# Kernel tuning notes

Measured on AMD Instinct MI355X. Metric: run time of the kernel, lower is better.

Reference implementation:

```python
import jax, jax.numpy as jnp
import numpy as np

N_NODES = 100000
N_EDGES = 1600000
IN_F = 128
HID = 128
N_CLASSES = 2
N_GRAPHS = 512


def setup_inputs() -> dict:
    key = jax.random.key(0)
    ks = jax.random.split(key, 12)
    x = jax.random.normal(ks[0], (N_NODES, IN_F), dtype=jnp.float32)
    edge_index = jax.random.randint(ks[1], (2, N_EDGES), 0, N_NODES, dtype=jnp.int64)
    batch = jnp.sort(jax.random.randint(ks[2], (N_NODES,), 0, N_GRAPHS, dtype=jnp.int64))
    s_in = 1.0 / np.sqrt(IN_F)
    s_h = 1.0 / np.sqrt(HID)
    return {
        "x": x,
        "edge_index": edge_index,
        "batch": batch,
        "W1": jax.random.normal(ks[3], (IN_F, HID), dtype=jnp.float32) * s_in,
        "b1": jnp.zeros((HID,), dtype=jnp.float32),
        "W2": jax.random.normal(ks[4], (HID, HID), dtype=jnp.float32) * s_h,
        "b2": jnp.zeros((HID,), dtype=jnp.float32),
        "W3": jax.random.normal(ks[5], (HID, HID), dtype=jnp.float32) * s_h,
        "b3": jnp.zeros((HID,), dtype=jnp.float32),
        "Wl": jax.random.normal(ks[6], (HID, N_CLASSES), dtype=jnp.float32) * s_h,
        "bl": jnp.zeros((N_CLASSES,), dtype=jnp.float32),
    }


def reference(x, edge_index, batch, W1, b1, W2, b2, W3, b3, Wl, bl):
    n = x.shape[0]
    src, dst = edge_index[0], edge_index[1]
    # GCNConv adds self-loops and applies symmetric normalization D^-1/2 (A+I) D^-1/2
    loop = jnp.arange(n, dtype=src.dtype)
    src_f = jnp.concatenate([src, loop])  # [E+N]
    dst_f = jnp.concatenate([dst, loop])
    deg = jax.ops.segment_sum(jnp.ones_like(src_f, dtype=x.dtype), dst_f, num_segments=n)
    dis = jax.lax.rsqrt(jnp.maximum(deg, 1.0))  # deg >= 1 due to self-loops
    norm = dis[src_f] * dis[dst_f]  # [E+N]

    def conv(h, W, b):
        h = h @ W                                    # [N, H]
        msg = h[src_f] * norm[:, None]               # gather + scale  [E+N, H]
        agg = jax.ops.segment_sum(msg, dst_f, num_segments=n)  # scatter-add
        return agg + b

    h = jax.nn.relu(conv(x, W1, b1))
    h = jax.nn.relu(conv(h, W2, b2))
    h = conv(h, W3, b3)
    # global_mean_pool over graph ids
    sums = jax.ops.segment_sum(h, batch, num_segments=N_GRAPHS)        # [G, H]
    cnt = jax.ops.segment_sum(jnp.ones((n,), h.dtype), batch, num_segments=N_GRAPHS)
    pooled = sums / jnp.maximum(cnt, 1.0)[:, None]
    # dropout p=0.5 is identity in eval mode
    return pooled @ Wl + bl
```

## Files before the change

kernel.cpp:

```cpp
#include <hip/hip_runtime.h>

#define NF 128
#define NFU 64
#define BW 128
#define KMAX 1024
#define CAP 3072
#define CHUNK 8192

typedef __attribute__((ext_vector_type(8))) short bf16x8;
typedef __attribute__((ext_vector_type(4))) float f32x4;
union U4S8 { uint4 u; bf16x8 s; };

__global__ void detect_kernel(const int* __restrict__ ei, int ne, int* __restrict__ mode) {
    if (threadIdx.x == 0 && blockIdx.x == 0) {
        int step = ne / 32; if (step < 1) step = 1;
        int all0 = 1;
        for (int k = 0; k < 16; ++k) {
            int idx = 2 * k * step + 1;
            if (ei[idx] != 0) { all0 = 0; break; }
        }
        *mode = all0;
    }
}

__global__ __launch_bounds__(256) void hist_kernel(const int* __restrict__ ei, int ne, int n,
                                                   const int* __restrict__ mode, int* __restrict__ btotal,
                                                   int K) {
    __shared__ int hist[KMAX];
    int m = *mode;
    int tid = threadIdx.x;
    for (int k = tid; k < K; k += 256) hist[k] = 0;
    __syncthreads();
    int base = blockIdx.x * CHUNK;
    int end = min(base + CHUNK, ne);
    for (int e = base + tid; e < end; e += 256) {
        int dst = m ? ei[2 * (ne + e)] : ei[ne + e];
        if ((unsigned)dst < (unsigned)n) atomicAdd(&hist[dst >> 7], 1);
    }
    __syncthreads();
    for (int k = tid; k < K; k += 256)
        if (hist[k]) atomicAdd(&btotal[k], hist[k]);
}

__global__ __launch_bounds__(1024) void scanK(const int* __restrict__ btotal, int* __restrict__ bbase,
                                              int* __restrict__ gcur, int K) {
    __shared__ int sm[1024];
    int tid = threadIdx.x;
    int v = (tid < K) ? btotal[tid] : 0;
    sm[tid] = v;
    __syncthreads();
    for (int off = 1; off < 1024; off <<= 1) {
        int t = (tid >= off) ? sm[tid - off] : 0;
        __syncthreads();
        sm[tid] += t;
        __syncthreads();
    }
    if (tid < K) {
        int excl = sm[tid] - v;
        bbase[tid] = excl;
        gcur[tid] = excl;
        if (tid == K - 1) bbase[K] = sm[tid];
    }
}

__global__ __launch_bounds__(256) void scatter_kernel(const int* __restrict__ ei, int ne, int n,
                                                      const int* __restrict__ mode, int* __restrict__ gcur,
                                                      uint2* __restrict__ pairbuf, int K) {
    __shared__ int cur[KMAX];
    int m = *mode;
    int tid = threadIdx.x;
    for (int k = tid; k < K; k += 256) cur[k] = 0;
    __syncthreads();
    int base = blockIdx.x * CHUNK;
    int end = min(base + CHUNK, ne);
    for (int e = base + tid; e < end; e += 256) {
        int dst = m ? ei[2 * (ne + e)] : ei[ne + e];
        if ((unsigned)dst < (unsigned)n) atomicAdd(&cur[dst >> 7], 1);
    }
    __syncthreads();
    for (int k = tid; k < K; k += 256) {
        int c = cur[k];
        cur[k] = c ? atomicAdd(&gcur[k], c) : 0;
    }
    __syncthreads();
    for (int e = base + tid; e < end; e += 256) {
        int src = m ? ei[2 * e] : ei[e];
        int dst = m ? ei[2 * (ne + e)] : ei[ne + e];
        if ((unsigned)dst >= (unsigned)n || (unsigned)src >= (unsigned)n) continue;
        int pos = atomicAdd(&cur[dst >> 7], 1);
        pairbuf[pos] = make_uint2((unsigned)src, (unsigned)dst);
    }
}

__global__ __launch_bounds__(256) void sort_kernel(const uint2* __restrict__ pairbuf,
                                                   const int* __restrict__ bbase,
                                                   int* __restrict__ rowptr, float* __restrict__ dis,
                                                   int* __restrict__ col, int n, int K) {
    __shared__ uint2 spair[CAP];
    __shared__ int lcol[CAP];
    __shared__ int dcnt[BW];
    __shared__ int pref[BW];
    int tid = threadIdx.x;
    int b = blockIdx.x;
    int r0 = b * BW;
    int base = bbase[b];
    int end = bbase[b + 1];
    int cntb = end - base;
    if (cntb > CAP) cntb = CAP;

    for (int i = tid; i < cntb; i += 256) spair[i] = pairbuf[base + i];
    if (tid < BW) dcnt[tid] = 0;
    __syncthreads();
    for (int i = tid; i < cntb; i += 256) atomicAdd(&dcnt[spair[i].y & (BW - 1)], 1);
    __syncthreads();
    if (tid < BW) pref[tid] = dcnt[tid];
    __syncthreads();
    for (int off = 1; off < BW; off <<= 1) {
        int t = (tid < BW && tid >= off) ? pref[tid - off] : 0;
        __syncthreads();
        if (tid < BW) pref[tid] += t;
        __syncthreads();
    }
    if (tid < BW) {
        int d = r0 + tid;
        if (d < n) {
            int excl = pref[tid] - dcnt[tid];
            rowptr[d] = base + excl;
            dis[d] = rsqrtf((float)(dcnt[tid] + 1));
        }
    }
    if (b == K - 1 && tid == 0) rowptr[n] = end;
    if (tid < BW) dcnt[tid] = pref[tid] - dcnt[tid];
    __syncthreads();
    for (int i = tid; i < cntb; i += 256) {
        int slot = atomicAdd(&dcnt[spair[i].y & (BW - 1)], 1);
        if (slot < CAP) lcol[slot] = (int)spair[i].x;
    }
    __syncthreads();
    for (int i = tid; i < cntb; i += 256) col[base + i] = lcol[i];
}

__device__ inline unsigned pack_bf16(float a, float b) {
    unsigned ua = __float_as_uint(a), ub = __float_as_uint(b);
    ua = (ua + 0x7fffu + ((ua >> 16) & 1u)) >> 16;
    ub = (ub + 0x7fffu + ((ub >> 16) & 1u)) >> 16;
    return ua | (ub << 16);
}
__device__ inline float bflo(unsigned u) { return __uint_as_float(u << 16); }
__device__ inline float bfhi(unsigned u) { return __uint_as_float(u & 0xFFFF0000u); }

__global__ __launch_bounds__(256) void wprep_kernel(const float* __restrict__ W, uint4* __restrict__ Wb) {
    int tid = threadIdx.x;
#pragma unroll
    for (int it = 0; it < 8; ++it) {
        int item = it * 256 + tid;
        int lane = item & 63;
        int kbjt = item >> 6;
        int kb = kbjt & 3, jt = kbjt >> 2;
        int k0 = kb * 32 + (lane >> 4) * 8;
        int j = jt * 16 + (lane & 15);
        unsigned p[4];
#pragma unroll
        for (int q = 0; q < 4; ++q)
            p[q] = pack_bf16(W[(size_t)(k0 + 2 * q) * NF + j], W[(size_t)(k0 + 2 * q + 1) * NF + j]);
        Wb[item] = make_uint4(p[0], p[1], p[2], p[3]);
    }
}

__global__ __launch_bounds__(256) void mm_mfma_kernel(const void* __restrict__ A, int a_fp32,
                                                      const uint4* __restrict__ Wb,
                                                      const float* __restrict__ dis,
                                                      unsigned* __restrict__ hs, int n) {
    int tid = threadIdx.x;
    int wave = tid >> 6, lane = tid & 63;
    int r0 = blockIdx.x * 64 + wave * 16;
    if (r0 >= n) return;
    int lrow = lane & 15, lk = lane >> 4;
    int arow = min(r0 + lrow, n - 1);

    f32x4 acc[8];
#pragma unroll
    for (int j = 0; j < 8; ++j) acc[j] = (f32x4){0.f, 0.f, 0.f, 0.f};

    U4S8 af[4];
    if (a_fp32) {
        const float* Af = (const float*)A;
#pragma unroll
        for (int kb = 0; kb < 4; ++kb) {
            const float* p = Af + (size_t)arow * NF + kb * 32 + lk * 8;
            float4 x0 = *(const float4*)p;
            float4 x1 = *(const float4*)(p + 4);
            af[kb].u = make_uint4(pack_bf16(x0.x, x0.y), pack_bf16(x0.z, x0.w),
                                  pack_bf16(x1.x, x1.y), pack_bf16(x1.z, x1.w));
        }
    } else {
        const unsigned* Ab = (const unsigned*)A;
#pragma unroll
        for (int kb = 0; kb < 4; ++kb)
            af[kb].u = *(const uint4*)(Ab + (size_t)arow * NFU + kb * 16 + lk * 4);
    }

#pragma unroll
    for (int kb = 0; kb < 4; ++kb) {
#pragma unroll
        for (int jt = 0; jt < 8; ++jt) {
            U4S8 wf;
            wf.u = Wb[(jt * 4 + kb) * 64 + lane];
            acc[jt] = __builtin_amdgcn_mfma_f32_16x16x32_bf16(wf.s, af[kb].s, acc[jt], 0, 0, 0);
        }
    }

    if (r0 + lrow < n) {
        float dv = dis[r0 + lrow];
        unsigned* orow = hs + (size_t)(r0 + lrow) * NFU;
#pragma unroll
        for (int jt = 0; jt < 8; ++jt) {
            unsigned p0 = pack_bf16(acc[jt][0] * dv, acc[jt][1] * dv);
            unsigned p1 = pack_bf16(acc[jt][2] * dv, acc[jt][3] * dv);
            *(uint2*)(orow + jt * 8 + lk * 2) = make_uint2(p0, p1);
        }
    }
}

__global__ __launch_bounds__(256) void spmm_kernel(const unsigned* __restrict__ hs, const int* __restrict__ rowptr,
                                                   const int* __restrict__ col, const float* __restrict__ dis,
                                                   const float* __restrict__ b, unsigned* __restrict__ outb,
                                                   int n, int do_relu) {
    int wid = (blockIdx.x * blockDim.x + threadIdx.x) >> 6;
    int lane = threadIdx.x & 63;
    if (wid >= n) return;
    int s = rowptr[wid], e = rowptr[wid + 1];
    int deg = e - s;
    int group = lane >> 4, fl = lane & 15;

    float acc[8];
    if (group == 0) {
        uint4 sv = *(const uint4*)(hs + (size_t)wid * NFU + fl * 4);
        acc[0] = bflo(sv.x); acc[1] = bfhi(sv.x);
        acc[2] = bflo(sv.y); acc[3] = bfhi(sv.y);
        acc[4] = bflo(sv.z); acc[5] = bfhi(sv.z);
        acc[6] = bflo(sv.w); acc[7] = bfhi(sv.w);
    } else {
#pragma unroll
        for (int k = 0; k < 8; ++k) acc[k] = 0.f;
    }

    int m64 = min(deg, 64);
    int cidx = (lane < m64) ? col[s + lane] : 0;

    for (int j0 = 0; j0 < m64; j0 += 4) {
        int c = __shfl(cidx, j0 + group);
        if (j0 + group < m64) {
            uint4 v = *(const uint4*)(hs + (size_t)c * NFU + fl * 4);
            acc[0] += bflo(v.x); acc[1] += bfhi(v.x);
            acc[2] += bflo(v.y); acc[3] += bfhi(v.y);
            acc[4] += bflo(v.z); acc[5] += bfhi(v.z);
            acc[6] += bflo(v.w); acc[7] += bfhi(v.w);
        }
    }
    for (int i = s + 64 + group; i < e; i += 4) {
        int c = col[i];
        uint4 v = *(const uint4*)(hs + (size_t)c * NFU + fl * 4);
        acc[0] += bflo(v.x); acc[1] += bfhi(v.x);
        acc[2] += bflo(v.y); acc[3] += bfhi(v.y);
        acc[4] += bflo(v.z); acc[5] += bfhi(v.z);
        acc[6] += bflo(v.w); acc[7] += bfhi(v.w);
    }

#pragma unroll
    for (int k = 0; k < 8; ++k) {
        acc[k] += __shfl_xor(acc[k], 16);
        acc[k] += __shfl_xor(acc[k], 32);
    }

    if (lane < 16) {
        float d = dis[wid];
        float4 bb0 = *(const float4*)(b + fl * 8);
        float4 bb1 = *(const float4*)(b + fl * 8 + 4);
        float o[8];
        o[0] = fmaf(d, acc[0], bb0.x); o[1] = fmaf(d, acc[1], bb0.y);
        o[2] = fmaf(d, acc[2], bb0.z); o[3] = fmaf(d, acc[3], bb0.w);
        o[4] = fmaf(d, acc[4], bb1.x); o[5] = fmaf(d, acc[5], bb1.y);
        o[6] = fmaf(d, acc[6], bb1.z); o[7] = fmaf(d, acc[7], bb1.w);
        if (do_relu) {
#pragma unroll
            for (int k = 0; k < 8; ++k) o[k] = fmaxf(o[k], 0.f);
        }
        unsigned q0 = pack_bf16(o[0], o[1]);
        unsigned q1 = pack_bf16(o[2], o[3]);
        unsigned q2 = pack_bf16(o[4], o[5]);
        unsigned q3 = pack_bf16(o[6], o[7]);
        *(uint4*)(outb + (size_t)wid * NFU + fl * 4) = make_uint4(q0, q1, q2, q3);
    }
}

__global__ void gbounds_kernel(const int* __restrict__ batch, const int* __restrict__ mode,
                               int* __restrict__ gstart, int n, int G) {
    int m = *mode;
    int i = blockIdx.x * blockDim.x + threadIdx.x;
    if (i >= n) return;
    int g1 = m ? batch[2 * i] : batch[i];
    int g2 = (i == n - 1) ? G : (m ? batch[2 * (i + 1)] : batch[i + 1]);
    if ((unsigned)g1 > (unsigned)G) g1 = G;
    if ((unsigned)g2 > (unsigned)G) g2 = G;
    if (i == 0) for (int g = 0; g <= g1; ++g) gstart[g] = 0;
    for (int g = g1 + 1; g <= g2; ++g) gstart[g] = i + 1;
}

__global__ __launch_bounds__(256) void poolhead_kernel(const unsigned* __restrict__ h, const int* __restrict__ gstart,
                                                       const float* __restrict__ Wl, const float* __restrict__ bl,
                                                       float* __restrict__ out, int G) {
    __shared__ float sacc[16][16][8];
    int g = blockIdx.x;
    int s = gstart[g], e = gstart[g + 1];
    int tid = threadIdx.x;
    int rg = tid >> 4, fl = tid & 15;

    float acc[8] = {0.f, 0.f, 0.f, 0.f, 0.f, 0.f, 0.f, 0.f};
    for (int i = s + rg; i < e; i += 16) {
        uint4 v = *(const uint4*)(h + (size_t)i * NFU + fl * 4);
        acc[0] += bflo(v.x); acc[1] += bfhi(v.x);
        acc[2] += bflo(v.y); acc[3] += bfhi(v.y);
        acc[4] += bflo(v.z); acc[5] += bfhi(v.z);
        acc[6] += bflo(v.w); acc[7] += bfhi(v.w);
    }
#pragma unroll
    for (int k = 0; k < 8; ++k) sacc[rg][fl][k] = acc[k];
    __syncthreads();
    if (tid < 16) {
        float t[8] = {0.f, 0.f, 0.f, 0.f, 0.f, 0.f, 0.f, 0.f};
        for (int r = 0; r < 16; ++r)
#pragma unroll
            for (int k = 0; k < 8; ++k) t[k] += sacc[r][tid][k];
        float inv = 1.0f / fmaxf((float)(e - s), 1.0f);
        float o0 = 0.f, o1 = 0.f;
#pragma unroll
        for (int k = 0; k < 8; ++k) {
            int f = tid * 8 + k;
            o0 += t[k] * inv * Wl[f * 2];
            o1 += t[k] * inv * Wl[f * 2 + 1];
        }
#pragma unroll
        for (int off2 = 8; off2; off2 >>= 1) {
            o0 += __shfl_down(o0, off2, 16);
            o1 += __shfl_down(o1, off2, 16);
        }
        if (tid == 0) {
            out[g * 2 + 0] = o0 + bl[0];
            out[g * 2 + 1] = o1 + bl[1];
        }
    }
}

extern "C" void kernel_launch(void* const* d_in, const int* in_sizes, int n_in,
                              void* d_out, int out_size, void* d_ws, size_t ws_size,
                              hipStream_t stream) {
    const float* x  = (const float*)d_in[0];
    const int*   ei = (const int*)d_in[1];
    const int*   bt = (const int*)d_in[2];
    const float* W1 = (const float*)d_in[3];
    const float* b1 = (const float*)d_in[4];
    const float* W2 = (const float*)d_in[5];
    const float* b2 = (const float*)d_in[6];
    const float* W3 = (const float*)d_in[7];
    const float* b3 = (const float*)d_in[8];
    const float* Wl = (const float*)d_in[9];
    const float* bl = (const float*)d_in[10];
    float* out = (float*)d_out;

    const int n  = in_sizes[2];
    const int ne = in_sizes[1] / 2;
    const int G  = out_size / 2;
    const int K  = (n + BW - 1) / BW;

    size_t off = 0;
    auto alloc = [&](size_t bytes) { size_t o = off; off += (bytes + 255) & ~(size_t)255; return o; };
    char* ws = (char*)d_ws;
    unsigned* hB     = (unsigned*)(ws + alloc((size_t)n * NFU * 4));
    unsigned* hsB    = (unsigned*)(ws + alloc((size_t)n * NFU * 4));
    uint2*    pairbuf= (uint2*)   (ws + alloc((size_t)ne * 8));
    int*      col    = (int*)     (ws + alloc((size_t)ne * 4));
    int*      rowptr = (int*)     (ws + alloc((size_t)(n + 1) * 4));
    float*    dis    = (float*)   (ws + alloc((size_t)n * 4));
    int*      btotal = (int*)     (ws + alloc((size_t)(K + 1) * 4));
    int*      bbase  = (int*)     (ws + alloc((size_t)(K + 1) * 4));
    int*      gcur   = (int*)     (ws + alloc((size_t)(K + 1) * 4));
    int*      gstart = (int*)     (ws + alloc((size_t)(G + 1) * 4));
    uint4*    Wb1    = (uint4*)   (ws + alloc(2048 * 16));
    uint4*    Wb2    = (uint4*)   (ws + alloc(2048 * 16));
    uint4*    Wb3    = (uint4*)   (ws + alloc(2048 * 16));
    int*      mode   = (int*)     (ws + alloc(256));
    (void)ws_size;

    const int nchunks = (ne + CHUNK - 1) / CHUNK;

    hipMemsetAsync(btotal, 0, (size_t)(K + 1) * 4, stream);

    detect_kernel<<<1, 64, 0, stream>>>(ei, ne, mode);

    wprep_kernel<<<1, 256, 0, stream>>>(W1, Wb1);
    wprep_kernel<<<1, 256, 0, stream>>>(W2, Wb2);
    wprep_kernel<<<1, 256, 0, stream>>>(W3, Wb3);

    hist_kernel<<<nchunks, 256, 0, stream>>>(ei, ne, n, mode, btotal, K);
    scanK<<<1, 1024, 0, stream>>>(btotal, bbase, gcur, K);
    scatter_kernel<<<nchunks, 256, 0, stream>>>(ei, ne, n, mode, gcur, pairbuf, K);
    sort_kernel<<<K, 256, 0, stream>>>(pairbuf, bbase, rowptr, dis, col, n, K);
    gbounds_kernel<<<(n + 255) / 256, 256, 0, stream>>>(bt, mode, gstart, n, G);

    const int mm_grid = (n + 63) / 64;
    const int sp_grid = (n + 3) / 4;

    mm_mfma_kernel<<<mm_grid, 256, 0, stream>>>(x, 1, Wb1, dis, hsB, n);
    spmm_kernel<<<sp_grid, 256, 0, stream>>>(hsB, rowptr, col, dis, b1, hB, n, 1);
    mm_mfma_kernel<<<mm_grid, 256, 0, stream>>>(hB, 0, Wb2, dis, hsB, n);
    spmm_kernel<<<sp_grid, 256, 0, stream>>>(hsB, rowptr, col, dis, b2, hB, n, 1);
    mm_mfma_kernel<<<mm_grid, 256, 0, stream>>>(hB, 0, Wb3, dis, hsB, n);
    spmm_kernel<<<sp_grid, 256, 0, stream>>>(hsB, rowptr, col, dis, b3, hB, n, 0);

    poolhead_kernel<<<G, 256, 0, stream>>>(hB, gstart, Wl, bl, out, G);
}
```

Before: 337.5 us.

## Reuse per-chunk histograms, pack edge pairs, unroll SpMM gathers, split pooling blocks

```diff
diff --git a/kernel.cpp b/kernel.cpp
--- a/kernel.cpp
+++ b/kernel.cpp
@@ -9,6 +9,7 @@
 
 typedef __attribute__((ext_vector_type(8))) short bf16x8;
 typedef __attribute__((ext_vector_type(4))) float f32x4;
+typedef __attribute__((ext_vector_type(2))) float f32x2;
 union U4S8 { uint4 u; bf16x8 s; };
 
 __global__ void detect_kernel(const int* __restrict__ ei, int ne, int* __restrict__ mode) {
@@ -25,7 +26,7 @@
 
 __global__ __launch_bounds__(256) void hist_kernel(const int* __restrict__ ei, int ne, int n,
                                                    const int* __restrict__ mode, int* __restrict__ btotal,
-                                                   int K) {
+                                                   int* __restrict__ blkcnt, int K) {
     __shared__ int hist[KMAX];
     int m = *mode;
     int tid = threadIdx.x;
@@ -38,8 +39,11 @@
         if ((unsigned)dst < (unsigned)n) atomicAdd(&hist[dst >> 7], 1);
     }
     __syncthreads();
-    for (int k = tid; k < K; k += 256)
-        if (hist[k]) atomicAdd(&btotal[k], hist[k]);
+    for (int k = tid; k < K; k += 256) {
+        int c = hist[k];
+        blkcnt[(size_t)blockIdx.x * K + k] = c;
+        if (c) atomicAdd(&btotal[k], c);
+    }
 }
 
 __global__ __launch_bounds__(1024) void scanK(const int* __restrict__ btotal, int* __restrict__ bbase,
@@ -64,39 +68,33 @@
 }
 
 __global__ __launch_bounds__(256) void scatter_kernel(const int* __restrict__ ei, int ne, int n,
-                                                      const int* __restrict__ mode, int* __restrict__ gcur,
-                                                      uint2* __restrict__ pairbuf, int K) {
+                                                      const int* __restrict__ mode, const int* __restrict__ blkcnt,
+                                                      int* __restrict__ gcur, unsigned* __restrict__ pairbuf,
+                                                      int K) {
     __shared__ int cur[KMAX];
     int m = *mode;
     int tid = threadIdx.x;
-    for (int k = tid; k < K; k += 256) cur[k] = 0;
+    for (int k = tid; k < K; k += 256) {
+        int c = blkcnt[(size_t)blockIdx.x * K + k];
+        cur[k] = c ? atomicAdd(&gcur[k], c) : 0;
+    }
     __syncthreads();
     int base = blockIdx.x * CHUNK;
     int end = min(base + CHUNK, ne);
-    for (int e = base + tid; e < end; e += 256) {
-        int dst = m ? ei[2 * (ne + e)] : ei[ne + e];
-        if ((unsigned)dst < (unsigned)n) atomicAdd(&cur[dst >> 7], 1);
-    }
-    __syncthreads();
-    for (int k = tid; k < K; k += 256) {
-        int c = cur[k];
-        cur[k] = c ? atomicAdd(&gcur[k], c) : 0;
-    }
-    __syncthreads();
     for (int e = base + tid; e < end; e += 256) {
         int src = m ? ei[2 * e] : ei[e];
         int dst = m ? ei[2 * (ne + e)] : ei[ne + e];
         if ((unsigned)dst >= (unsigned)n || (unsigned)src >= (unsigned)n) continue;
         int pos = atomicAdd(&cur[dst >> 7], 1);
-        pairbuf[pos] = make_uint2((unsigned)src, (unsigned)dst);
-    }
-}
-
-__global__ __launch_bounds__(256) void sort_kernel(const uint2* __restrict__ pairbuf,
+        pairbuf[pos] = (unsigned)src | ((unsigned)(dst & (BW - 1)) << 24);
+    }
+}
+
+__global__ __launch_bounds__(256) void sort_kernel(const unsigned* __restrict__ pairbuf,
                                                    const int* __restrict__ bbase,
                                                    int* __restrict__ rowptr, float* __restrict__ dis,
                                                    int* __restrict__ col, int n, int K) {
-    __shared__ uint2 spair[CAP];
+    __shared__ unsigned spair[CAP];
     __shared__ int lcol[CAP];
     __shared__ int dcnt[BW];
     __shared__ int pref[BW];
@@ -111,7 +109,7 @@
     for (int i = tid; i < cntb; i += 256) spair[i] = pairbuf[base + i];
     if (tid < BW) dcnt[tid] = 0;
     __syncthreads();
-    for (int i = tid; i < cntb; i += 256) atomicAdd(&dcnt[spair[i].y & (BW - 1)], 1);
+    for (int i = tid; i < cntb; i += 256) atomicAdd(&dcnt[spair[i] >> 24], 1);
     __syncthreads();
     if (tid < BW) pref[tid] = dcnt[tid];
     __syncthreads();
@@ -133,8 +131,9 @@
     if (tid < BW) dcnt[tid] = pref[tid] - dcnt[tid];
     __syncthreads();
     for (int i = tid; i < cntb; i += 256) {
-        int slot = atomicAdd(&dcnt[spair[i].y & (BW - 1)], 1);
-        if (slot < CAP) lcol[slot] = (int)spair[i].x;
+        unsigned p = spair[i];
+        int slot = atomicAdd(&dcnt[p >> 24], 1);
+        if (slot < CAP) lcol[slot] = (int)(p & 0xFFFFFFu);
     }
     __syncthreads();
     for (int i = tid; i < cntb; i += 256) col[base + i] = lcol[i];
@@ -149,7 +148,10 @@
 __device__ inline float bflo(unsigned u) { return __uint_as_float(u << 16); }
 __device__ inline float bfhi(unsigned u) { return __uint_as_float(u & 0xFFFF0000u); }
 
-__global__ __launch_bounds__(256) void wprep_kernel(const float* __restrict__ W, uint4* __restrict__ Wb) {
+__global__ __launch_bounds__(256) void wprep3_kernel(const float* __restrict__ W1, const float* __restrict__ W2,
+                                                     const float* __restrict__ W3, uint4* __restrict__ Wb) {
+    const float* W = (blockIdx.x == 0) ? W1 : (blockIdx.x == 1) ? W2 : W3;
+    uint4* o = Wb + (size_t)blockIdx.x * 2048;
     int tid = threadIdx.x;
 #pragma unroll
     for (int it = 0; it < 8; ++it) {
@@ -163,7 +165,7 @@
 #pragma unroll
         for (int q = 0; q < 4; ++q)
             p[q] = pack_bf16(W[(size_t)(k0 + 2 * q) * NF + j], W[(size_t)(k0 + 2 * q + 1) * NF + j]);
-        Wb[item] = make_uint4(p[0], p[1], p[2], p[3]);
+        o[item] = make_uint4(p[0], p[1], p[2], p[3]);
     }
 }
 
@@ -221,6 +223,12 @@
         }
     }
 }
+
+#define SPACC(v)                                              \
+    { a0 += (f32x2){bflo((v).x), bfhi((v).x)};                \
+      a1 += (f32x2){bflo((v).y), bfhi((v).y)};                \
+      a2 += (f32x2){bflo((v).z), bfhi((v).z)};                \
+      a3 += (f32x2){bflo((v).w), bfhi((v).w)}; }
 
 __global__ __launch_bounds__(256) void spmm_kernel(const unsigned* __restrict__ hs, const int* __restrict__ rowptr,
                                                    const int* __restrict__ col, const float* __restrict__ dis,
@@ -233,44 +241,44 @@
     int deg = e - s;
     int group = lane >> 4, fl = lane & 15;
 
-    float acc[8];
+    f32x2 a0 = {0.f, 0.f}, a1 = {0.f, 0.f}, a2 = {0.f, 0.f}, a3 = {0.f, 0.f};
     if (group == 0) {
         uint4 sv = *(const uint4*)(hs + (size_t)wid * NFU + fl * 4);
-        acc[0] = bflo(sv.x); acc[1] = bfhi(sv.x);
-        acc[2] = bflo(sv.y); acc[3] = bfhi(sv.y);
-        acc[4] = bflo(sv.z); acc[5] = bfhi(sv.z);
-        acc[6] = bflo(sv.w); acc[7] = bfhi(sv.w);
-    } else {
-#pragma unroll
-        for (int k = 0; k < 8; ++k) acc[k] = 0.f;
+        SPACC(sv);
     }
 
     int m64 = min(deg, 64);
     int cidx = (lane < m64) ? col[s + lane] : 0;
 
-    for (int j0 = 0; j0 < m64; j0 += 4) {
-        int c = __shfl(cidx, j0 + group);
-        if (j0 + group < m64) {
+    int j0 = 0;
+    for (; j0 + 8 <= m64; j0 += 8) {
+        int ca = __shfl(cidx, j0 + group);
+        int cb = __shfl(cidx, j0 + 4 + group);
+        uint4 va = *(const uint4*)(hs + (size_t)ca * NFU + fl * 4);
+        uint4 vb = *(const uint4*)(hs + (size_t)cb * NFU + fl * 4);
+        SPACC(va);
+        SPACC(vb);
+    }
+    for (; j0 < m64; j0 += 4) {
+        int jj = j0 + group;
+        int c = __shfl(cidx, jj);
+        if (jj < m64) {
             uint4 v = *(const uint4*)(hs + (size_t)c * NFU + fl * 4);
-            acc[0] += bflo(v.x); acc[1] += bfhi(v.x);
-            acc[2] += bflo(v.y); acc[3] += bfhi(v.y);
-            acc[4] += bflo(v.z); acc[5] += bfhi(v.z);
-            acc[6] += bflo(v.w); acc[7] += bfhi(v.w);
+            SPACC(v);
         }
     }
     for (int i = s + 64 + group; i < e; i += 4) {
         int c = col[i];
         uint4 v = *(const uint4*)(hs + (size_t)c * NFU + fl * 4);
-        acc[0] += bflo(v.x); acc[1] += bfhi(v.x);
-        acc[2] += bflo(v.y); acc[3] += bfhi(v.y);
-        acc[4] += bflo(v.z); acc[5] += bfhi(v.z);
-        acc[6] += bflo(v.w); acc[7] += bfhi(v.w);
-    }
-
-#pragma unroll
-    for (int k = 0; k < 8; ++k) {
-        acc[k] += __shfl_xor(acc[k], 16);
-        acc[k] += __shfl_xor(acc[k], 32);
+        SPACC(v);
+    }
+
+#pragma unroll
+    for (int k = 0; k < 2; ++k) {
+        a0[k] += __shfl_xor(a0[k], 16); a0[k] += __shfl_xor(a0[k], 32);
+        a1[k] += __shfl_xor(a1[k], 16); a1[k] += __shfl_xor(a1[k], 32);
+        a2[k] += __shfl_xor(a2[k], 16); a2[k] += __shfl_xor(a2[k], 32);
+        a3[k] += __shfl_xor(a3[k], 16); a3[k] += __shfl_xor(a3[k], 32);
     }
 
     if (lane < 16) {
@@ -278,10 +286,10 @@
         float4 bb0 = *(const float4*)(b + fl * 8);
         float4 bb1 = *(const float4*)(b + fl * 8 + 4);
         float o[8];
-        o[0] = fmaf(d, acc[0], bb0.x); o[1] = fmaf(d, acc[1], bb0.y);
-        o[2] = fmaf(d, acc[2], bb0.z); o[3] = fmaf(d, acc[3], bb0.w);
-        o[4] = fmaf(d, acc[4], bb1.x); o[5] = fmaf(d, acc[5], bb1.y);
-        o[6] = fmaf(d, acc[6], bb1.z); o[7] = fmaf(d, acc[7], bb1.w);
+        o[0] = fmaf(d, a0[0], bb0.x); o[1] = fmaf(d, a0[1], bb0.y);
+        o[2] = fmaf(d, a1[0], bb0.z); o[3] = fmaf(d, a1[1], bb0.w);
+        o[4] = fmaf(d, a2[0], bb1.x); o[5] = fmaf(d, a2[1], bb1.y);
+        o[6] = fmaf(d, a3[0], bb1.z); o[7] = fmaf(d, a3[1], bb1.w);
         if (do_relu) {
 #pragma unroll
             for (int k = 0; k < 8; ++k) o[k] = fmaxf(o[k], 0.f);
@@ -311,8 +319,12 @@
                                                        const float* __restrict__ Wl, const float* __restrict__ bl,
                                                        float* __restrict__ out, int G) {
     __shared__ float sacc[16][16][8];
-    int g = blockIdx.x;
-    int s = gstart[g], e = gstart[g + 1];
+    int g = blockIdx.x >> 2, sub = blockIdx.x & 3;
+    int s0 = gstart[g], e0 = gstart[g + 1];
+    int cnt = e0 - s0;
+    int per = (cnt + 3) >> 2;
+    int s = s0 + sub * per;
+    int e = min(s + per, e0);
     int tid = threadIdx.x;
     int rg = tid >> 4, fl = tid & 15;
 
@@ -332,7 +344,7 @@
         for (int r = 0; r < 16; ++r)
 #pragma unroll
             for (int k = 0; k < 8; ++k) t[k] += sacc[r][tid][k];
-        float inv = 1.0f / fmaxf((float)(e - s), 1.0f);
+        float inv = 1.0f / fmaxf((float)cnt, 1.0f);
         float o0 = 0.f, o1 = 0.f;
 #pragma unroll
         for (int k = 0; k < 8; ++k) {
@@ -346,8 +358,9 @@
             o1 += __shfl_down(o1, off2, 16);
         }
         if (tid == 0) {
-            out[g * 2 + 0] = o0 + bl[0];
-            out[g * 2 + 1] = o1 + bl[1];
+            if (sub == 0) { o0 += bl[0]; o1 += bl[1]; }
+            atomicAdd(&out[g * 2 + 0], o0);
+            atomicAdd(&out[g * 2 + 1], o1);
         }
     }
 }
@@ -372,13 +385,14 @@
     const int ne = in_sizes[1] / 2;
     const int G  = out_size / 2;
     const int K  = (n + BW - 1) / BW;
+    const int nchunks = (ne + CHUNK - 1) / CHUNK;
 
     size_t off = 0;
     auto alloc = [&](size_t bytes) { size_t o = off; off += (bytes + 255) & ~(size_t)255; return o; };
     char* ws = (char*)d_ws;
     unsigned* hB     = (unsigned*)(ws + alloc((size_t)n * NFU * 4));
     unsigned* hsB    = (unsigned*)(ws + alloc((size_t)n * NFU * 4));
-    uint2*    pairbuf= (uint2*)   (ws + alloc((size_t)ne * 8));
+    unsigned* pairbuf= (unsigned*)(ws + alloc((size_t)ne * 4));
     int*      col    = (int*)     (ws + alloc((size_t)ne * 4));
     int*      rowptr = (int*)     (ws + alloc((size_t)(n + 1) * 4));
     float*    dis    = (float*)   (ws + alloc((size_t)n * 4));
@@ -386,37 +400,32 @@
     int*      bbase  = (int*)     (ws + alloc((size_t)(K + 1) * 4));
     int*      gcur   = (int*)     (ws + alloc((size_t)(K + 1) * 4));
     int*      gstart = (int*)     (ws + alloc((size_t)(G + 1) * 4));
-    uint4*    Wb1    = (uint4*)   (ws + alloc(2048 * 16));
-    uint4*    Wb2    = (uint4*)   (ws + alloc(2048 * 16));
-    uint4*    Wb3    = (uint4*)   (ws + alloc(2048 * 16));
+    int*      blkcnt = (int*)     (ws + alloc((size_t)nchunks * K * 4));
+    uint4*    Wb     = (uint4*)   (ws + alloc(3 * 2048 * 16));
     int*      mode   = (int*)     (ws + alloc(256));
     (void)ws_size;
 
-    const int nchunks = (ne + CHUNK - 1) / CHUNK;
-
     hipMemsetAsync(btotal, 0, (size_t)(K + 1) * 4, stream);
+    hipMemsetAsync(out, 0, (size_t)out_size * 4, stream);
 
     detect_kernel<<<1, 64, 0, stream>>>(ei, ne, mode);
-
-    wprep_kernel<<<1, 256, 0, stream>>>(W1, Wb1);
-    wprep_kernel<<<1, 256, 0, stream>>>(W2, Wb2);
-    wprep_kernel<<<1, 256, 0, stream>>>(W3, Wb3);
-
-    hist_kernel<<<nchunks, 256, 0, stream>>>(ei, ne, n, mode, btotal, K);
+    wprep3_kernel<<<3, 256, 0, stream>>>(W1, W2, W3, Wb);
+
+    hist_kernel<<<nchunks, 256, 0, stream>>>(ei, ne, n, mode, btotal, blkcnt, K);
     scanK<<<1, 1024, 0, stream>>>(btotal, bbase, gcur, K);
-    scatter_kernel<<<nchunks, 256, 0, stream>>>(ei, ne, n, mode, gcur, pairbuf, K);
+    scatter_kernel<<<nchunks, 256, 0, stream>>>(ei, ne, n, mode, blkcnt, gcur, pairbuf, K);
     sort_kernel<<<K, 256, 0, stream>>>(pairbuf, bbase, rowptr, dis, col, n, K);
     gbounds_kernel<<<(n + 255) / 256, 256, 0, stream>>>(bt, mode, gstart, n, G);
 
     const int mm_grid = (n + 63) / 64;
     const int sp_grid = (n + 3) / 4;
 
-    mm_mfma_kernel<<<mm_grid, 256, 0, stream>>>(x, 1, Wb1, dis, hsB, n);
+    mm_mfma_kernel<<<mm_grid, 256, 0, stream>>>(x, 1, Wb, dis, hsB, n);
     spmm_kernel<<<sp_grid, 256, 0, stream>>>(hsB, rowptr, col, dis, b1, hB, n, 1);
-    mm_mfma_kernel<<<mm_grid, 256, 0, stream>>>(hB, 0, Wb2, dis, hsB, n);
+    mm_mfma_kernel<<<mm_grid, 256, 0, stream>>>(hB, 0, Wb + 2048, dis, hsB, n);
     spmm_kernel<<<sp_grid, 256, 0, stream>>>(hsB, rowptr, col, dis, b2, hB, n, 1);
-    mm_mfma_kernel<<<mm_grid, 256, 0, stream>>>(hB, 0, Wb3, dis, hsB, n);
+    mm_mfma_kernel<<<mm_grid, 256, 0, stream>>>(hB, 0, Wb + 4096, dis, hsB, n);
     spmm_kernel<<<sp_grid, 256, 0, stream>>>(hsB, rowptr, col, dis, b3, hB, n, 0);
 
-    poolhead_kernel<<<G, 256, 0, stream>>>(hB, gstart, Wl, bl, out, G);
-}
+    poolhead_kernel<<<G * 4, 256, 0, stream>>>(hB, gstart, Wl, bl, out, G);
+}
```

After: 321.3 us. 4.8% less time.
